# Performance work log

Measured on AMD Instinct MI355X. Metric: run time of the kernel, lower is better.

## Reference

```python
import jax, jax.numpy as jnp
import numpy as np

N_GRAPHS = 64
NODES_PER_GRAPH = 1024
N_NODES = N_GRAPHS * NODES_PER_GRAPH
AVG_DEGREE = 32
N_EDGES = N_NODES * AVG_DEGREE
D_FEAT = 256
ALPHA = 0.5
RATIO = 0.5
K = max(int(RATIO * NODES_PER_GRAPH), 1)  # 512 kept nodes per graph


def setup_inputs() -> dict:
    key = jax.random.key(0)
    ks = jax.random.split(key, 6)
    x = jax.random.normal(ks[0], (N_NODES, D_FEAT), dtype=jnp.float32)
    # intra-graph random edges (src, dst local in [0, n), offset by graph id)
    epg = N_EDGES // N_GRAPHS
    src_loc = jax.random.randint(ks[1], (N_EDGES,), 0, NODES_PER_GRAPH, dtype=jnp.int32)
    dst_loc = jax.random.randint(ks[2], (N_EDGES,), 0, NODES_PER_GRAPH, dtype=jnp.int32)
    off = (jnp.arange(N_EDGES, dtype=jnp.int32) // epg) * NODES_PER_GRAPH
    edge_index = jnp.stack([src_loc + off, dst_loc + off])  # [2, E] int32
    batch = jnp.repeat(jnp.arange(N_GRAPHS, dtype=jnp.int32), NODES_PER_GRAPH)
    scale = 1.0 / np.sqrt(D_FEAT)
    w1 = jax.random.normal(ks[3], (D_FEAT, 1), dtype=jnp.float32) * scale
    b1 = jnp.zeros((1,), dtype=jnp.float32)
    wg = jax.random.normal(ks[4], (D_FEAT, 1), dtype=jnp.float32) * scale
    bg = jnp.zeros((1,), dtype=jnp.float32)
    return {"x": x, "edge_index": edge_index, "batch": batch,
            "w1": w1, "b1": b1, "wg": wg, "bg": bg}


def reference(x, edge_index, batch, w1, b1, wg, bg):
    N = x.shape[0]
    row, col = edge_index[0], edge_index[1]
    # remove_self_loops only affects the GCN scoring path
    ew = (row != col).astype(x.dtype)  # zero-weight self loops == removed
    # GCNConv (add_self_loops=False): D^-1/2 A D^-1/2 (X Wg) + bg
    deg = jnp.zeros((N,), x.dtype).at[col].add(ew)
    dis = jnp.where(deg > 0, jax.lax.rsqrt(jnp.maximum(deg, 1.0)), 0.0)
    norm = dis[row] * dis[col] * ew  # [E]
    xw = x @ wg  # [N, 1]
    gcn = jnp.zeros((N, 1), x.dtype).at[col].add(norm[:, None] * xw[row]) + bg
    score = (ALPHA * (x @ w1 + b1) + (1.0 - ALPHA) * gcn).squeeze(-1)  # [N]
    # segmented top-k: equal-sized graphs -> reshape to [B, n]
    sc = score.reshape(N_GRAPHS, NODES_PER_GRAPH)
    _, idx = jax.lax.top_k(sc, K)  # [B, K], descending (matches torch.topk order)
    perm = (idx + (jnp.arange(N_GRAPHS, dtype=idx.dtype) * NODES_PER_GRAPH)[:, None]).reshape(-1)
    x_new = x[perm] * jnp.tanh(score[perm])[:, None]  # [B*K, D]
    batch_new = batch[perm]
    # filter_adj: keep edges with both endpoints selected, relabel by position in perm
    node_map = jnp.full((N,), -1, jnp.int32).at[perm].set(jnp.arange(perm.shape[0], dtype=jnp.int32))
    er, ec = node_map[row], node_map[col]
    valid = (er >= 0) & (ec >= 0)
    new_edge_index = jnp.where(valid[None, :], jnp.stack([er, ec]), -1)  # -1 marks dropped edges
    return x_new, new_edge_index, batch_new
```

## Files before the change

### kernel.cpp

```cpp
#include <hip/hip_runtime.h>

#define NPG 1024
#define NG 64
#define KKEEP 512
#define DF 256
#define NTOT (NG * NPG)
#define NROWS (NG * KKEEP)
#define EPG 32768
#define NBD 4
#define EPBD (EPG / NBD)
#define NB 8
#define EPB (EPG / NB)
#define HI_ROWS 256
#define LO_ROWS (NROWS - HI_ROWS)
#define FXS 1099511627776.0

typedef float vf4 __attribute__((ext_vector_type(4)));
typedef int   vi4 __attribute__((ext_vector_type(4)));

__device__ __forceinline__ unsigned long long cex(unsigned long long a, int t, int k, int j) {
    unsigned long long b = __shfl_xor(a, j, 64);
    bool lower = ((t & j) == 0);
    bool desc  = ((t & k) == 0);
    unsigned long long mn = a < b ? a : b;
    unsigned long long mx = a < b ? b : a;
    return (desc == lower) ? mx : mn;
}

__global__ __launch_bounds__(256) void k_front(const float* __restrict__ x,
                                               const float* __restrict__ w1,
                                               const float* __restrict__ wg,
                                               const int* __restrict__ rows,
                                               const int* __restrict__ cols,
                                               float* __restrict__ sc0,
                                               float* __restrict__ xwg,
                                               int* __restrict__ degp) {
    __shared__ int deg_l[NPG];
    const int b = blockIdx.x;
    const int t = threadIdx.x;
    if (b < NTOT / 4) {
        int node = b * 4 + (t >> 6);
        int lane = t & 63;
        const float4 xv = *reinterpret_cast<const float4*>(x + (size_t)node * DF + lane * 4);
        const float4 av = *reinterpret_cast<const float4*>(w1 + lane * 4);
        const float4 bv = *reinterpret_cast<const float4*>(wg + lane * 4);
        double s1 = (double)xv.x * av.x + (double)xv.y * av.y + (double)xv.z * av.z + (double)xv.w * av.w;
        double s2 = (double)xv.x * bv.x + (double)xv.y * bv.y + (double)xv.z * bv.z + (double)xv.w * bv.w;
#pragma unroll
        for (int off = 32; off; off >>= 1) {
            s1 += __shfl_xor(s1, off);
            s2 += __shfl_xor(s2, off);
        }
        if (lane == 0) { sc0[node] = (float)s1; xwg[node] = (float)s2; }
    } else {
        const int bb = b - NTOT / 4;
        const int g = bb >> 2, sub = bb & 3;
        deg_l[t] = 0; deg_l[t + 256] = 0; deg_l[t + 512] = 0; deg_l[t + 768] = 0;
        __syncthreads();
        const int4* r4 = reinterpret_cast<const int4*>(rows + (size_t)g * EPG + sub * EPBD);
        const int4* c4 = reinterpret_cast<const int4*>(cols + (size_t)g * EPG + sub * EPBD);
#pragma unroll 2
        for (int i = t; i < EPBD / 4; i += 256) {
            int4 r = r4[i], c = c4[i];
            if (r.x != c.x) atomicAdd(&deg_l[c.x & (NPG - 1)], 1);
            if (r.y != c.y) atomicAdd(&deg_l[c.y & (NPG - 1)], 1);
            if (r.z != c.z) atomicAdd(&deg_l[c.z & (NPG - 1)], 1);
            if (r.w != c.w) atomicAdd(&deg_l[c.w & (NPG - 1)], 1);
        }
        __syncthreads();
        int* dst = degp + (size_t)bb * NPG;
        dst[t] = deg_l[t]; dst[t + 256] = deg_l[t + 256];
        dst[t + 512] = deg_l[t + 512]; dst[t + 768] = deg_l[t + 768];
    }
}

__global__ __launch_bounds__(1024) void k_gcn(const int* __restrict__ rows,
                                              const int* __restrict__ cols,
                                              const int* __restrict__ degp,
                                              const float* __restrict__ xwg,
                                              unsigned long long* __restrict__ gcnp) {
    __shared__ float dis_l[NPG];
    __shared__ float dxw_l[NPG];
    __shared__ unsigned long long gcn_l[NPG];
    const int t = threadIdx.x;
    const int g = blockIdx.x >> 3, sub = blockIdx.x & 7;
    {
        int d = degp[(size_t)(g * NBD + 0) * NPG + t] + degp[(size_t)(g * NBD + 1) * NPG + t]
              + degp[(size_t)(g * NBD + 2) * NPG + t] + degp[(size_t)(g * NBD + 3) * NPG + t];
        float dis = (d > 0) ? (1.0f / sqrtf((float)d)) : 0.0f;
        dis_l[t] = dis;
        dxw_l[t] = dis * xwg[g * NPG + t];
    }
    gcn_l[t] = 0;
    __syncthreads();
    const int4* r4 = reinterpret_cast<const int4*>(rows + (size_t)g * EPG + sub * EPB);
    const int4* c4 = reinterpret_cast<const int4*>(cols + (size_t)g * EPG + sub * EPB);
    for (int i = t; i < EPB / 4; i += 1024) {
        int4 r = r4[i], c = c4[i];
        int rl, cl; float term;
        rl = r.x & (NPG - 1); cl = c.x & (NPG - 1);
        if (r.x != c.x) { term = dxw_l[rl] * dis_l[cl];
            atomicAdd(&gcn_l[cl], (unsigned long long)(long long)llrint((double)term * FXS)); }
        rl = r.y & (NPG - 1); cl = c.y & (NPG - 1);
        if (r.y != c.y) { term = dxw_l[rl] * dis_l[cl];
            atomicAdd(&gcn_l[cl], (unsigned long long)(long long)llrint((double)term * FXS)); }
        rl = r.z & (NPG - 1); cl = c.z & (NPG - 1);
        if (r.z != c.z) { term = dxw_l[rl] * dis_l[cl];
            atomicAdd(&gcn_l[cl], (unsigned long long)(long long)llrint((double)term * FXS)); }
        rl = r.w & (NPG - 1); cl = c.w & (NPG - 1);
        if (r.w != c.w) { term = dxw_l[rl] * dis_l[cl];
            atomicAdd(&gcn_l[cl], (unsigned long long)(long long)llrint((double)term * FXS)); }
    }
    __syncthreads();
    gcnp[(size_t)blockIdx.x * NPG + t] = gcn_l[t];
}

__global__ __launch_bounds__(1024) void k_sort(const float* __restrict__ sc0,
                                               const unsigned long long* __restrict__ gcnp,
                                               const float* __restrict__ b1,
                                               const float* __restrict__ bg,
                                               int* __restrict__ node_map,
                                               int2* __restrict__ rowinfo) {
    __shared__ unsigned long long keys[NPG];
    __shared__ float score_l[NPG];
    const int g = blockIdx.x, t = threadIdx.x;
    const int nbase = g * NPG;
    unsigned long long key;
    {
        long long q = 0;
#pragma unroll
        for (int p = 0; p < NB; ++p) q += (long long)gcnp[(size_t)(g * NB + p) * NPG + t];
        float s2 = (float)((double)q * (1.0 / FXS)) + bg[0];
        float s1 = sc0[nbase + t] + b1[0];
        float s = 0.5f * s1 + 0.5f * s2;
        score_l[t] = s;
        unsigned u = __float_as_uint(s);
        u = (u & 0x80000000u) ? ~u : (u | 0x80000000u);
        key = ((unsigned long long)u << 32) | (unsigned long long)(0xFFFFFFFFu - (unsigned)t);
    }
#pragma unroll
    for (int k = 2; k <= 64; k <<= 1)
        for (int j = k >> 1; j > 0; j >>= 1)
            key = cex(key, t, k, j);
    keys[t] = key;
    __syncthreads();
    for (int k = 128; k <= NPG; k <<= 1) {
        for (int j = k >> 1; j >= 64; j >>= 1) {
            int ixj = t ^ j;
            if (ixj > t) {
                unsigned long long a = keys[t], b = keys[ixj];
                bool desc = ((t & k) == 0);
                if (desc ? (a < b) : (a > b)) { keys[t] = b; keys[ixj] = a; }
            }
            __syncthreads();
        }
        key = keys[t];
#pragma unroll
        for (int j = 32; j > 0; j >>= 1)
            key = cex(key, t, k, j);
        if (k < NPG) { keys[t] = key; __syncthreads(); }
    }
    int idx = (int)(0xFFFFFFFFu - (unsigned)(key & 0xFFFFFFFFull)) & (NPG - 1);
    if (t < KKEEP) {
        int row = g * KKEEP + t;
        node_map[nbase + idx] = row;
        rowinfo[row] = make_int2(nbase + idx, __float_as_int(tanhf(score_l[idx])));
    } else {
        node_map[nbase + idx] = -1;
    }
}

__device__ __forceinline__ void edge_body(const int* __restrict__ rows,
                                          const int* __restrict__ cols,
                                          const int* __restrict__ node_map,
                                          float* __restrict__ oute, int E, int i) {
    vi4 r = __builtin_nontemporal_load(reinterpret_cast<const vi4*>(rows) + i);
    vi4 c = __builtin_nontemporal_load(reinterpret_cast<const vi4*>(cols) + i);
    int ex = node_map[r.x & (NTOT - 1)], fx = node_map[c.x & (NTOT - 1)];
    int ey = node_map[r.y & (NTOT - 1)], fy = node_map[c.y & (NTOT - 1)];
    int ez = node_map[r.z & (NTOT - 1)], fz = node_map[c.z & (NTOT - 1)];
    int ew = node_map[r.w & (NTOT - 1)], fw = node_map[c.w & (NTOT - 1)];
    vf4 orow, ocol;
    orow.x = (ex >= 0 && fx >= 0) ? (float)ex : -1.0f;  ocol.x = (ex >= 0 && fx >= 0) ? (float)fx : -1.0f;
    orow.y = (ey >= 0 && fy >= 0) ? (float)ey : -1.0f;  ocol.y = (ey >= 0 && fy >= 0) ? (float)fy : -1.0f;
    orow.z = (ez >= 0 && fz >= 0) ? (float)ez : -1.0f;  ocol.z = (ez >= 0 && fz >= 0) ? (float)fz : -1.0f;
    orow.w = (ew >= 0 && fw >= 0) ? (float)ew : -1.0f;  ocol.w = (ew >= 0 && fw >= 0) ? (float)fw : -1.0f;
    __builtin_nontemporal_store(orow, reinterpret_cast<vf4*>(oute) + i);
    __builtin_nontemporal_store(ocol, reinterpret_cast<vf4*>(oute + (size_t)E) + i);
}

__device__ __forceinline__ void gather_row(const float* __restrict__ x, int2 ri, int row,
                                           float* __restrict__ outx, float* __restrict__ outb,
                                           int lane) {
    float tg = __int_as_float(ri.y);
    const float4 v = *reinterpret_cast<const float4*>(x + (size_t)(ri.x & (NTOT - 1)) * DF + lane * 4);
    vf4 o;
    o.x = v.x * tg; o.y = v.y * tg; o.z = v.z * tg; o.w = v.w * tg;
    __builtin_nontemporal_store(o, reinterpret_cast<vf4*>(outx + (size_t)row * DF) + lane);
    if (lane == 0) __builtin_nontemporal_store((float)(row >> 9), outb + row);
}

__global__ __launch_bounds__(256) void k_out(const float* __restrict__ x,
                                             const int* __restrict__ rows,
                                             const int* __restrict__ cols,
                                             const int* __restrict__ node_map,
                                             const int2* __restrict__ rowinfo,
                                             float* __restrict__ outx,
                                             float* __restrict__ oute,
                                             float* __restrict__ outb, int E) {
    const int b = blockIdx.x, t = threadIdx.x;
    if (b < NROWS / 4) {
        int row = b * 4 + (t >> 6);
        gather_row(x, rowinfo[row], row, outx, outb, t & 63);
    } else {
        int i = (b - NROWS / 4) * 256 + t;
        if (i < E / 4) edge_body(rows, cols, node_map, oute, E, i);
    }
}

__global__ __launch_bounds__(256) void k_edges(const int* __restrict__ rows,
                                               const int* __restrict__ cols,
                                               const int* __restrict__ node_map,
                                               float* __restrict__ oute, int E) {
    int i = blockIdx.x * blockDim.x + threadIdx.x;
    if (i < E / 4) edge_body(rows, cols, node_map, oute, E, i);
}

__global__ __launch_bounds__(256) void k_gather(const float* __restrict__ x,
                                                const int2* __restrict__ rowinfo,
                                                float* __restrict__ outx,
                                                float* __restrict__ outb) {
    int row = blockIdx.x * 4 + (threadIdx.x >> 6);
    gather_row(x, rowinfo[row], row, outx, outb, threadIdx.x & 63);
}

__global__ __launch_bounds__(1024) void k_gather_hi(const float* __restrict__ x,
                                                    const int2* __restrict__ rowinfo,
                                                    float* __restrict__ outx,
                                                    float* __restrict__ outb) {
    __shared__ int2 info[HI_ROWS];
    int tid = threadIdx.x;
    if (tid < HI_ROWS) info[tid] = rowinfo[LO_ROWS + tid];
    __syncthreads();
    for (int it = tid; it < HI_ROWS * 64; it += 1024) {
        int rl = it >> 6, lane = it & 63;
        gather_row(x, info[rl], LO_ROWS + rl, outx, outb, lane);
    }
}

extern "C" void kernel_launch(void* const* d_in, const int* in_sizes, int n_in,
                              void* d_out, int out_size, void* d_ws, size_t ws_size,
                              hipStream_t stream) {
    const float* x = (const float*)d_in[0];
    const int* ei = (const int*)d_in[1];
    const float* w1 = (const float*)d_in[3];
    const float* b1 = (const float*)d_in[4];
    const float* wg = (const float*)d_in[5];
    const float* bg = (const float*)d_in[6];

    const int N = in_sizes[0] / DF;
    const int E = in_sizes[1] / 2;
    const int* rows = ei;
    const int* cols = ei + E;

    float* outx = (float*)d_out;
    float* oute = outx + (size_t)NROWS * DF;
    float* outb = oute + (size_t)2 * E;

    char* sb = (char*)d_out;
    float*              sc0  = (float*)(sb + 0);
    float*              xwg  = (float*)(sb + (1 << 18));
    int*                degp = (int*)(sb + (2 << 18));
    unsigned long long* gcnp = (unsigned long long*)(sb + (6 << 18));

    int tier;
    int*  node_map;
    int2* rowinfo;
    if (ws_size >= (size_t)(NTOT * 4 + NROWS * 8)) {
        tier = 1;
        node_map = (int*)d_ws;
        rowinfo  = (int2*)((char*)d_ws + (size_t)NTOT * 4);
    } else if (ws_size >= (size_t)(NROWS * 8)) {
        tier = 2;
        node_map = (int*)(sb + (22 << 18));
        rowinfo  = (int2*)d_ws;
    } else {
        tier = 3;
        node_map = (int*)(sb + (22 << 18));
        rowinfo  = (int2*)(sb + (size_t)NROWS * DF * 4 - (size_t)NROWS * 8);
    }

    hipLaunchKernelGGL(k_front, dim3(NTOT / 4 + NG * NBD), dim3(256), 0, stream,
                       x, w1, wg, rows, cols, sc0, xwg, degp);
    hipLaunchKernelGGL(k_gcn, dim3(NG * NB), dim3(1024), 0, stream, rows, cols, degp, xwg, gcnp);
    hipLaunchKernelGGL(k_sort, dim3(NG), dim3(1024), 0, stream, sc0, gcnp, b1, bg, node_map, rowinfo);
    if (tier == 1) {
        hipLaunchKernelGGL(k_out, dim3(NROWS / 4 + E / 4 / 256), dim3(256), 0, stream,
                           x, rows, cols, node_map, rowinfo, outx, oute, outb, E);
    } else if (tier == 2) {
        hipLaunchKernelGGL(k_edges, dim3(E / 4 / 256), dim3(256), 0, stream, rows, cols, node_map, oute, E);
        hipLaunchKernelGGL(k_gather, dim3(NROWS / 4), dim3(256), 0, stream, x, rowinfo, outx, outb);
    } else {
        hipLaunchKernelGGL(k_edges, dim3(E / 4 / 256), dim3(256), 0, stream, rows, cols, node_map, oute, E);
        hipLaunchKernelGGL(k_gather, dim3(LO_ROWS / 4), dim3(256), 0, stream, x, rowinfo, outx, outb);
        hipLaunchKernelGGL(k_gather_hi, dim3(1), dim3(1024), 0, stream, x, rowinfo, outx, outb);
    }
}
```

Measured before the change: 62.97 us.

## Pack local edge endpoints into one word reused by GCN and edge-filter passes

The degree pass now also writes each edge as a single 32-bit word holding its local source and destination indices. The GCN scatter and the edge-filter pass read this packed array instead of the two separate int arrays, which halves their edge-index read traffic. The dot-product part of the front kernel is reorganised so each 16-lane group handles one node over four float4 chunks, giving 16 nodes per block instead of 4. The cost is an extra write of the packed array and more scratch space, which now sits in the workspace or the output buffer depending on workspace size.

```diff
diff --git a/kernel.cpp b/kernel.cpp
--- a/kernel.cpp
+++ b/kernel.cpp
@@ -14,9 +14,11 @@
 #define HI_ROWS 256
 #define LO_ROWS (NROWS - HI_ROWS)
 #define FXS 1099511627776.0
+#define DOTS_BLOCKS (NTOT / 16)
 
 typedef float vf4 __attribute__((ext_vector_type(4)));
 typedef int   vi4 __attribute__((ext_vector_type(4)));
+typedef unsigned int vu4 __attribute__((ext_vector_type(4)));
 
 __device__ __forceinline__ unsigned long long cex(unsigned long long a, int t, int k, int j) {
     unsigned long long b = __shfl_xor(a, j, 64);
@@ -34,38 +36,53 @@
                                                const int* __restrict__ cols,
                                                float* __restrict__ sc0,
                                                float* __restrict__ xwg,
-                                               int* __restrict__ degp) {
+                                               int* __restrict__ degp,
+                                               unsigned int* __restrict__ ep) {
     __shared__ int deg_l[NPG];
     const int b = blockIdx.x;
     const int t = threadIdx.x;
-    if (b < NTOT / 4) {
-        int node = b * 4 + (t >> 6);
-        int lane = t & 63;
-        const float4 xv = *reinterpret_cast<const float4*>(x + (size_t)node * DF + lane * 4);
-        const float4 av = *reinterpret_cast<const float4*>(w1 + lane * 4);
-        const float4 bv = *reinterpret_cast<const float4*>(wg + lane * 4);
-        double s1 = (double)xv.x * av.x + (double)xv.y * av.y + (double)xv.z * av.z + (double)xv.w * av.w;
-        double s2 = (double)xv.x * bv.x + (double)xv.y * bv.y + (double)xv.z * bv.z + (double)xv.w * bv.w;
-#pragma unroll
-        for (int off = 32; off; off >>= 1) {
-            s1 += __shfl_xor(s1, off);
-            s2 += __shfl_xor(s2, off);
-        }
-        if (lane == 0) { sc0[node] = (float)s1; xwg[node] = (float)s2; }
-    } else {
-        const int bb = b - NTOT / 4;
+    if (b < DOTS_BLOCKS) {
+        const int lane = t & 63;
+        const int grp  = lane & 15;
+        const int node = b * 16 + (t >> 6) * 4 + (lane >> 4);
+        double s1 = 0.0, s2 = 0.0;
+#pragma unroll
+        for (int i = 0; i < 4; ++i) {
+            const int off = grp * 4 + i * 64;
+            const float4 xv = *reinterpret_cast<const float4*>(x + (size_t)node * DF + off);
+            const float4 av = *reinterpret_cast<const float4*>(w1 + off);
+            const float4 bv = *reinterpret_cast<const float4*>(wg + off);
+            s1 += (double)xv.x * av.x + (double)xv.y * av.y + (double)xv.z * av.z + (double)xv.w * av.w;
+            s2 += (double)xv.x * bv.x + (double)xv.y * bv.y + (double)xv.z * bv.z + (double)xv.w * bv.w;
+        }
+#pragma unroll
+        for (int m = 1; m <= 8; m <<= 1) {
+            s1 += __shfl_xor(s1, m);
+            s2 += __shfl_xor(s2, m);
+        }
+        if (grp == 0) { sc0[node] = (float)s1; xwg[node] = (float)s2; }
+    } else {
+        const int bb = b - DOTS_BLOCKS;
         const int g = bb >> 2, sub = bb & 3;
         deg_l[t] = 0; deg_l[t + 256] = 0; deg_l[t + 512] = 0; deg_l[t + 768] = 0;
         __syncthreads();
-        const int4* r4 = reinterpret_cast<const int4*>(rows + (size_t)g * EPG + sub * EPBD);
-        const int4* c4 = reinterpret_cast<const int4*>(cols + (size_t)g * EPG + sub * EPBD);
+        const size_t e0 = (size_t)g * EPG + sub * EPBD;
+        const int4* r4 = reinterpret_cast<const int4*>(rows + e0);
+        const int4* c4 = reinterpret_cast<const int4*>(cols + e0);
+        vu4* ep4 = reinterpret_cast<vu4*>(ep + e0);
 #pragma unroll 2
         for (int i = t; i < EPBD / 4; i += 256) {
             int4 r = r4[i], c = c4[i];
-            if (r.x != c.x) atomicAdd(&deg_l[c.x & (NPG - 1)], 1);
-            if (r.y != c.y) atomicAdd(&deg_l[c.y & (NPG - 1)], 1);
-            if (r.z != c.z) atomicAdd(&deg_l[c.z & (NPG - 1)], 1);
-            if (r.w != c.w) atomicAdd(&deg_l[c.w & (NPG - 1)], 1);
+            vu4 p;
+            p.x = (((unsigned)r.x & (NPG - 1)) << 10) | ((unsigned)c.x & (NPG - 1));
+            p.y = (((unsigned)r.y & (NPG - 1)) << 10) | ((unsigned)c.y & (NPG - 1));
+            p.z = (((unsigned)r.z & (NPG - 1)) << 10) | ((unsigned)c.z & (NPG - 1));
+            p.w = (((unsigned)r.w & (NPG - 1)) << 10) | ((unsigned)c.w & (NPG - 1));
+            ep4[i] = p;
+            if (r.x != c.x) atomicAdd(&deg_l[p.x & (NPG - 1)], 1);
+            if (r.y != c.y) atomicAdd(&deg_l[p.y & (NPG - 1)], 1);
+            if (r.z != c.z) atomicAdd(&deg_l[p.z & (NPG - 1)], 1);
+            if (r.w != c.w) atomicAdd(&deg_l[p.w & (NPG - 1)], 1);
         }
         __syncthreads();
         int* dst = degp + (size_t)bb * NPG;
@@ -74,8 +91,7 @@
     }
 }
 
-__global__ __launch_bounds__(1024) void k_gcn(const int* __restrict__ rows,
-                                              const int* __restrict__ cols,
+__global__ __launch_bounds__(1024) void k_gcn(const unsigned int* __restrict__ ep,
                                               const int* __restrict__ degp,
                                               const float* __restrict__ xwg,
                                               unsigned long long* __restrict__ gcnp) {
@@ -93,22 +109,21 @@
     }
     gcn_l[t] = 0;
     __syncthreads();
-    const int4* r4 = reinterpret_cast<const int4*>(rows + (size_t)g * EPG + sub * EPB);
-    const int4* c4 = reinterpret_cast<const int4*>(cols + (size_t)g * EPG + sub * EPB);
+    const vu4* ep4 = reinterpret_cast<const vu4*>(ep + (size_t)g * EPG + sub * EPB);
     for (int i = t; i < EPB / 4; i += 1024) {
-        int4 r = r4[i], c = c4[i];
+        vu4 p = ep4[i];
         int rl, cl; float term;
-        rl = r.x & (NPG - 1); cl = c.x & (NPG - 1);
-        if (r.x != c.x) { term = dxw_l[rl] * dis_l[cl];
+        rl = (p.x >> 10) & (NPG - 1); cl = p.x & (NPG - 1);
+        if (rl != cl) { term = dxw_l[rl] * dis_l[cl];
             atomicAdd(&gcn_l[cl], (unsigned long long)(long long)llrint((double)term * FXS)); }
-        rl = r.y & (NPG - 1); cl = c.y & (NPG - 1);
-        if (r.y != c.y) { term = dxw_l[rl] * dis_l[cl];
+        rl = (p.y >> 10) & (NPG - 1); cl = p.y & (NPG - 1);
+        if (rl != cl) { term = dxw_l[rl] * dis_l[cl];
             atomicAdd(&gcn_l[cl], (unsigned long long)(long long)llrint((double)term * FXS)); }
-        rl = r.z & (NPG - 1); cl = c.z & (NPG - 1);
-        if (r.z != c.z) { term = dxw_l[rl] * dis_l[cl];
+        rl = (p.z >> 10) & (NPG - 1); cl = p.z & (NPG - 1);
+        if (rl != cl) { term = dxw_l[rl] * dis_l[cl];
             atomicAdd(&gcn_l[cl], (unsigned long long)(long long)llrint((double)term * FXS)); }
-        rl = r.w & (NPG - 1); cl = c.w & (NPG - 1);
-        if (r.w != c.w) { term = dxw_l[rl] * dis_l[cl];
+        rl = (p.w >> 10) & (NPG - 1); cl = p.w & (NPG - 1);
+        if (rl != cl) { term = dxw_l[rl] * dis_l[cl];
             atomicAdd(&gcn_l[cl], (unsigned long long)(long long)llrint((double)term * FXS)); }
     }
     __syncthreads();
@@ -170,10 +185,28 @@
     }
 }
 
-__device__ __forceinline__ void edge_body(const int* __restrict__ rows,
-                                          const int* __restrict__ cols,
-                                          const int* __restrict__ node_map,
-                                          float* __restrict__ oute, int E, int i) {
+__device__ __forceinline__ void edge_body_packed(const unsigned int* __restrict__ ep,
+                                                 const int* __restrict__ node_map,
+                                                 float* __restrict__ oute, int E, int i) {
+    const int* nm = node_map + (i >> 13) * NPG;
+    vu4 p = __builtin_nontemporal_load(reinterpret_cast<const vu4*>(ep) + i);
+    int ex = nm[(p.x >> 10) & (NPG - 1)], fx = nm[p.x & (NPG - 1)];
+    int ey = nm[(p.y >> 10) & (NPG - 1)], fy = nm[p.y & (NPG - 1)];
+    int ez = nm[(p.z >> 10) & (NPG - 1)], fz = nm[p.z & (NPG - 1)];
+    int ew = nm[(p.w >> 10) & (NPG - 1)], fw = nm[p.w & (NPG - 1)];
+    vf4 orow, ocol;
+    orow.x = (ex >= 0 && fx >= 0) ? (float)ex : -1.0f;  ocol.x = (ex >= 0 && fx >= 0) ? (float)fx : -1.0f;
+    orow.y = (ey >= 0 && fy >= 0) ? (float)ey : -1.0f;  ocol.y = (ey >= 0 && fy >= 0) ? (float)fy : -1.0f;
+    orow.z = (ez >= 0 && fz >= 0) ? (float)ez : -1.0f;  ocol.z = (ez >= 0 && fz >= 0) ? (float)fz : -1.0f;
+    orow.w = (ew >= 0 && fw >= 0) ? (float)ew : -1.0f;  ocol.w = (ew >= 0 && fw >= 0) ? (float)fw : -1.0f;
+    __builtin_nontemporal_store(orow, reinterpret_cast<vf4*>(oute) + i);
+    __builtin_nontemporal_store(ocol, reinterpret_cast<vf4*>(oute + (size_t)E) + i);
+}
+
+__device__ __forceinline__ void edge_body_raw(const int* __restrict__ rows,
+                                              const int* __restrict__ cols,
+                                              const int* __restrict__ node_map,
+                                              float* __restrict__ oute, int E, int i) {
     vi4 r = __builtin_nontemporal_load(reinterpret_cast<const vi4*>(rows) + i);
     vi4 c = __builtin_nontemporal_load(reinterpret_cast<const vi4*>(cols) + i);
     int ex = node_map[r.x & (NTOT - 1)], fx = node_map[c.x & (NTOT - 1)];
@@ -201,6 +234,7 @@
 }
 
 __global__ __launch_bounds__(256) void k_out(const float* __restrict__ x,
+                                             const unsigned int* __restrict__ ep,
                                              const int* __restrict__ rows,
                                              const int* __restrict__ cols,
                                              const int* __restrict__ node_map,
@@ -214,16 +248,18 @@
         gather_row(x, rowinfo[row], row, outx, outb, t & 63);
     } else {
         int i = (b - NROWS / 4) * 256 + t;
-        if (i < E / 4) edge_body(rows, cols, node_map, oute, E, i);
-    }
-}
-
-__global__ __launch_bounds__(256) void k_edges(const int* __restrict__ rows,
-                                               const int* __restrict__ cols,
+        if (i < E / 4) {
+            if (ep) edge_body_packed(ep, node_map, oute, E, i);
+            else    edge_body_raw(rows, cols, node_map, oute, E, i);
+        }
+    }
+}
+
+__global__ __launch_bounds__(256) void k_edges(const unsigned int* __restrict__ ep,
                                                const int* __restrict__ node_map,
                                                float* __restrict__ oute, int E) {
     int i = blockIdx.x * blockDim.x + threadIdx.x;
-    if (i < E / 4) edge_body(rows, cols, node_map, oute, E, i);
+    if (i < E / 4) edge_body_packed(ep, node_map, oute, E, i);
 }
 
 __global__ __launch_bounds__(256) void k_gather(const float* __restrict__ x,
@@ -273,35 +309,50 @@
     int*                degp = (int*)(sb + (2 << 18));
     unsigned long long* gcnp = (unsigned long long*)(sb + (6 << 18));
 
+    const size_t EPBYTES = (size_t)E * 4;
     int tier;
     int*  node_map;
     int2* rowinfo;
-    if (ws_size >= (size_t)(NTOT * 4 + NROWS * 8)) {
+    unsigned int* ep;
+    unsigned int* ep_out;
+    if (ws_size >= (size_t)NTOT * 4 + (size_t)NROWS * 8 + EPBYTES) {
         tier = 1;
         node_map = (int*)d_ws;
         rowinfo  = (int2*)((char*)d_ws + (size_t)NTOT * 4);
-    } else if (ws_size >= (size_t)(NROWS * 8)) {
+        ep       = (unsigned int*)((char*)d_ws + (size_t)NTOT * 4 + (size_t)NROWS * 8);
+        ep_out   = ep;
+    } else if (ws_size >= (size_t)NTOT * 4 + (size_t)NROWS * 8) {
+        tier = 1;
+        node_map = (int*)d_ws;
+        rowinfo  = (int2*)((char*)d_ws + (size_t)NTOT * 4);
+        ep       = (unsigned int*)(sb + (22 << 18));
+        ep_out   = nullptr;
+    } else if (ws_size >= (size_t)NROWS * 8) {
         tier = 2;
-        node_map = (int*)(sb + (22 << 18));
+        node_map = (int*)(sb + (54 << 18));
         rowinfo  = (int2*)d_ws;
+        ep       = (unsigned int*)(sb + (22 << 18));
+        ep_out   = ep;
     } else {
         tier = 3;
-        node_map = (int*)(sb + (22 << 18));
+        node_map = (int*)(sb + (54 << 18));
         rowinfo  = (int2*)(sb + (size_t)NROWS * DF * 4 - (size_t)NROWS * 8);
-    }
-
-    hipLaunchKernelGGL(k_front, dim3(NTOT / 4 + NG * NBD), dim3(256), 0, stream,
-                       x, w1, wg, rows, cols, sc0, xwg, degp);
-    hipLaunchKernelGGL(k_gcn, dim3(NG * NB), dim3(1024), 0, stream, rows, cols, degp, xwg, gcnp);
+        ep       = (unsigned int*)(sb + (22 << 18));
+        ep_out   = ep;
+    }
+
+    hipLaunchKernelGGL(k_front, dim3(DOTS_BLOCKS + NG * NBD), dim3(256), 0, stream,
+                       x, w1, wg, rows, cols, sc0, xwg, degp, ep);
+    hipLaunchKernelGGL(k_gcn, dim3(NG * NB), dim3(1024), 0, stream, ep, degp, xwg, gcnp);
     hipLaunchKernelGGL(k_sort, dim3(NG), dim3(1024), 0, stream, sc0, gcnp, b1, bg, node_map, rowinfo);
     if (tier == 1) {
         hipLaunchKernelGGL(k_out, dim3(NROWS / 4 + E / 4 / 256), dim3(256), 0, stream,
-                           x, rows, cols, node_map, rowinfo, outx, oute, outb, E);
+                           x, ep_out, rows, cols, node_map, rowinfo, outx, oute, outb, E);
     } else if (tier == 2) {
-        hipLaunchKernelGGL(k_edges, dim3(E / 4 / 256), dim3(256), 0, stream, rows, cols, node_map, oute, E);
+        hipLaunchKernelGGL(k_edges, dim3(E / 4 / 256), dim3(256), 0, stream, ep_out, node_map, oute, E);
         hipLaunchKernelGGL(k_gather, dim3(NROWS / 4), dim3(256), 0, stream, x, rowinfo, outx, outb);
     } else {
-        hipLaunchKernelGGL(k_edges, dim3(E / 4 / 256), dim3(256), 0, stream, rows, cols, node_map, oute, E);
+        hipLaunchKernelGGL(k_edges, dim3(E / 4 / 256), dim3(256), 0, stream, ep_out, node_map, oute, E);
         hipLaunchKernelGGL(k_gather, dim3(LO_ROWS / 4), dim3(256), 0, stream, x, rowinfo, outx, outb);
         hipLaunchKernelGGL(k_gather_hi, dim3(1), dim3(1024), 0, stream, x, rowinfo, outx, outb);
     }
```

Result: faster. 52.67 us (-16.4%).
